# Optimization experiments

Hardware: AMD Instinct MI355X
Metric: run time of the kernel (lower is better)

The kernel has to match this reference:

```python
import jax, jax.numpy as jnp
import numpy as np

CUTOFF = 5.0
ENV_EXP = 5          # envelope_exponent
NUM_RADIAL = 6
EMB = 128
NUM_ATOM_TYPES = 95
N_NODES = 50000
N_EDGES = 800000


def envelope(x):
    # p = exponent + 1
    p = ENV_EXP + 1
    a = -(p + 1) * (p + 2) / 2.0
    b = p * (p + 2) * 1.0
    c = -p * (p + 1) / 2.0
    x_p_0 = x ** (p - 1)
    x_p_1 = x_p_0 * x
    x_p_2 = x_p_1 * x
    return 1.0 / x + a * x_p_0 + b * x_p_1 + c * x_p_2


def setup_inputs() -> dict:
    key = jax.random.key(0)
    ks = jax.random.split(key, 10)
    Z = jax.random.randint(ks[0], (N_NODES,), 0, NUM_ATOM_TYPES)
    src = jax.random.randint(ks[1], (N_EDGES,), 0, N_NODES)
    dst = jax.random.randint(ks[2], (N_EDGES,), 0, N_NODES)
    rbf = jax.random.normal(ks[3], (N_EDGES, NUM_RADIAL), dtype=jnp.float32)
    # distances in (0, cutoff]; keep away from 0 to avoid 1/x blowup
    d = jax.random.uniform(ks[4], (N_EDGES,), dtype=jnp.float32,
                           minval=0.05, maxval=1.0) * CUTOFF
    sqrt3 = float(np.sqrt(3.0))
    emb_table = jax.random.uniform(ks[5], (NUM_ATOM_TYPES, EMB),
                                   dtype=jnp.float32, minval=-sqrt3, maxval=sqrt3)
    W_rbf = jax.random.normal(ks[6], (EMB, NUM_RADIAL), dtype=jnp.float32) * (1.0 / np.sqrt(NUM_RADIAL))
    b_rbf = jnp.zeros((EMB,), dtype=jnp.float32)
    W_dense = jax.random.normal(ks[7], (EMB, 3 * EMB), dtype=jnp.float32) * (1.0 / np.sqrt(3 * EMB))
    b_dense = jnp.zeros((EMB,), dtype=jnp.float32)
    return {"Z": Z, "src": src, "dst": dst, "rbf": rbf, "d": d,
            "emb_table": emb_table, "W_rbf": W_rbf, "b_rbf": b_rbf,
            "W_dense": W_dense, "b_dense": b_dense}


def reference(Z, src, dst, rbf, d, emb_table, W_rbf, b_rbf, W_dense, b_dense):
    act = jax.nn.silu
    # node embeddings: g.ndata['h'] = embedding(Z)
    h = emb_table[Z]                                   # [N, EMB]
    # edge_init
    rbf_proj = act(rbf @ W_rbf.T + b_rbf)              # [E, EMB]
    m = jnp.concatenate([h[src], h[dst], rbf_proj], axis=-1)  # [E, 3*EMB]
    m = act(m @ W_dense.T + b_dense)                   # [E, EMB]
    d_scaled = d / CUTOFF                              # [E]
    # bessel funcs: sin(n*pi*x)/x, n = 1..NUM_RADIAL (stacked along dim=1)
    freqs = jnp.pi * jnp.arange(1, NUM_RADIAL + 1, dtype=d.dtype)  # [R]
    rbf_env = jnp.sin(d_scaled[:, None] * freqs) / d_scaled[:, None]  # [E, R]
    d_cutoff = envelope(d_scaled)                      # [E]
    rbf_env = d_cutoff[:, None] * rbf_env              # [E, R]
    return h, m, rbf_env
```

## Files before the change

kernel.cpp:

```cpp
#include <hip/hip_runtime.h>
#include <hip/hip_bf16.h>
#include <math.h>

#define CUTOFFV 5.0f
#define NRAD 6
#define EMB 128
#define NTYPES 95
#define PI_F 3.14159265358979323846f

typedef short short8 __attribute__((ext_vector_type(8)));
typedef float f32x4 __attribute__((ext_vector_type(4)));
typedef float f32x2 __attribute__((ext_vector_type(2)));

__device__ __forceinline__ unsigned short f2bf(float f) {
    union { float f; unsigned int u; } v; v.f = f;
    unsigned int u = v.u;
    unsigned int r = (u + 0x7FFFu + ((u >> 16) & 1u)) >> 16;
    return (unsigned short)r;
}

__device__ __forceinline__ short bf16s(float f) {
    union { __hip_bfloat16 h; short s; } u;
    u.h = __float2bfloat16(f);
    return u.s;
}

__device__ __forceinline__ float fast_rcp(float x) {
    float y;
    asm("v_rcp_f32 %0, %1" : "=v"(y) : "v"(x));
    return y;
}

__device__ __forceinline__ float silu_f(float x) {
    return x * fast_rcp(1.0f + __expf(-x));
}

__device__ __forceinline__ void lds_barrier() {
    __builtin_amdgcn_sched_barrier(0);
    asm volatile("s_waitcnt lgkmcnt(0)\n\ts_barrier" ::: "memory");
    __builtin_amdgcn_sched_barrier(0);
}

__global__ void prep_kernel(const float* __restrict__ emb,
                            const float* __restrict__ Wd,
                            const float* __restrict__ bd,
                            const float* __restrict__ Wr,
                            const float* __restrict__ brbf,
                            float* __restrict__ P1, float* __restrict__ P2,
                            unsigned short* __restrict__ W3b,
                            float* __restrict__ Wrp) {
    int b = blockIdx.x, tid = threadIdx.x;
    if (b < 2 * NTYPES) {
        int t = b / NTYPES, z = b % NTYPES;
        __shared__ float emb_s[EMB];
        emb_s[tid] = emb[z * EMB + tid];
        __syncthreads();
        float acc = (t == 0) ? bd[tid] : 0.0f;
        const float* wrow = Wd + (size_t)tid * 384 + t * EMB;
        #pragma unroll 8
        for (int j = 0; j < EMB; ++j) acc += emb_s[j] * wrow[j];
        (t == 0 ? P1 : P2)[z * EMB + tid] = acc;
    } else if (b < 2 * NTYPES + 8) {
        int g = (b - 2 * NTYPES) * 128 + tid;
        for (int i = g; i < EMB * EMB; i += 8 * 128) {
            int n = i >> 7, k = i & 127;
            W3b[i] = f2bf(Wd[(size_t)n * 384 + 256 + k]);
        }
    } else {
        if (tid < EMB) {
            int k = tid;
            #pragma unroll
            for (int j = 0; j < 6; ++j) Wrp[k * 8 + j] = Wr[k * 6 + j];
            Wrp[k * 8 + 6] = brbf[k];
            Wrp[k * 8 + 7] = 0.0f;
        }
    }
}

__global__ void h_kernel(const int* __restrict__ Z, const float* __restrict__ emb,
                         float* __restrict__ out_h, int N) {
    int idx = blockIdx.x * 256 + threadIdx.x;
    int total = N * (EMB / 4);
    if (idx >= total) return;
    int v = idx >> 5, c = idx & 31;
    int z = Z[v];
    const f32x4* e4 = (const f32x4*)emb;
    f32x4* o4 = (f32x4*)out_h;
    o4[idx] = e4[z * 32 + c];
}

__global__ void env_kernel(const float* __restrict__ dvec,
                           float* __restrict__ out_env, int E) {
    int e = blockIdx.x * 256 + threadIdx.x;
    if (e >= E) return;
    float x = dvec[e] * (1.0f / CUTOFFV);
    float inv = fast_rcp(x);
    float x2 = x * x;
    float x5 = x2 * x2 * x;
    float env = inv + x5 * (-28.0f + x * (48.0f - 21.0f * x));
    float s1, c1;
    __sincosf(PI_F * x, &s1, &c1);
    float twoc = 2.0f * c1;
    float f = env * inv;
    float s2 = twoc * s1;
    float s3 = twoc * s2 - s1;
    float s4 = twoc * s3 - s2;
    float s5 = twoc * s4 - s3;
    float s6 = twoc * s5 - s4;
    float* o = out_env + (size_t)e * 6;
    __builtin_nontemporal_store((f32x2){f * s1, f * s2}, (f32x2*)o);
    __builtin_nontemporal_store((f32x2){f * s3, f * s4}, (f32x2*)(o + 2));
    __builtin_nontemporal_store((f32x2){f * s5, f * s6}, (f32x2*)(o + 4));
}

__global__ void __launch_bounds__(256, 4)
edge_kernel(const int* __restrict__ Z, const int* __restrict__ src,
            const int* __restrict__ dst, const float* __restrict__ rbf,
            const float* __restrict__ P1, const float* __restrict__ P2,
            const unsigned short* __restrict__ W3b,
            const float* __restrict__ Wrp,
            float* __restrict__ out_m,
            int E, int ntiles) {
    __shared__ unsigned char A_lds[2][64 * 256];
    __shared__ int zs_s[2][64], zd_s[2][64];

    const int tid = threadIdx.x;
    const int lane = tid & 63;
    const int w = tid >> 6;
    const int lr = lane & 15;
    const int lg = lane >> 4;
    const int wu = __builtin_amdgcn_readfirstlane(w);

    short8 wfrag[2][4];
    #pragma unroll
    for (int nt = 0; nt < 2; ++nt) {
        int n = w * 32 + nt * 16 + lr;
        #pragma unroll
        for (int ks = 0; ks < 4; ++ks)
            wfrag[nt][ks] = *(const short8*)(W3b + n * EMB + ks * 32 + lg * 8);
    }

    for (int i = 0; ; ++i) {
        const int tp = blockIdx.x + i * gridDim.x;
        const int tc = tp - gridDim.x;
        const bool do_p = (tp < ntiles);
        const bool do_c = (i > 0) && (tc < ntiles);
        if (!do_p && !do_c) break;
        const int pi = i & 1, ci = pi ^ 1;

        f32x2 ra = {0.f, 0.f}, rb = {0.f, 0.f}, rc = {0.f, 0.f};
        int iv = 0;
        if (do_p) {
            const int e0p = tp * 64;
            int ecl = e0p + lane; if (ecl >= E) ecl = E - 1;
            const f32x2* r2 = (const f32x2*)(rbf + (size_t)ecl * 6);
            ra = r2[0]; rb = r2[1]; rc = r2[2];
            if (tid < 128) {
                int ec = e0p + (tid & 63); if (ec >= E) ec = E - 1;
                iv = (tid < 64) ? src[ec] : dst[ec];
            }
        }

        if (do_c) {
            const int e0c = tc * 64;
            const unsigned char* Ab = A_lds[ci];
            #pragma unroll
            for (int et = 0; et < 4; ++et) {
                const int e_row = et * 16 + lr;
                short8 bfrag[4];
                #pragma unroll
                for (int ks = 0; ks < 4; ++ks) {
                    int off = (e_row * 256 + (ks * 32 + lg * 8) * 2) ^ ((e_row & 7) << 4);
                    bfrag[ks] = *(const short8*)(Ab + off);
                }
                f32x4 acc[2];
                acc[0] = (f32x4){0.f, 0.f, 0.f, 0.f};
                acc[1] = (f32x4){0.f, 0.f, 0.f, 0.f};
                #pragma unroll
                for (int ks = 0; ks < 4; ++ks)
                    #pragma unroll
                    for (int nt = 0; nt < 2; ++nt)
                        acc[nt] = __builtin_amdgcn_mfma_f32_16x16x32_bf16(
                            wfrag[nt][ks], bfrag[ks], acc[nt], 0, 0, 0);

                const int el = e_row;
                const int e = e0c + el;
                const int zs = zs_s[ci][el], zd = zd_s[ci][el];
                #pragma unroll
                for (int nt = 0; nt < 2; ++nt) {
                    int n4 = w * 32 + nt * 16 + lg * 4;
                    const f32x4 p1 = *(const f32x4*)(P1 + zs * EMB + n4);
                    const f32x4 p2 = *(const f32x4*)(P2 + zd * EMB + n4);
                    f32x4 o;
                    o.x = silu_f(acc[nt][0] + p1.x + p2.x);
                    o.y = silu_f(acc[nt][1] + p1.y + p2.y);
                    o.z = silu_f(acc[nt][2] + p1.z + p2.z);
                    o.w = silu_f(acc[nt][3] + p1.w + p2.w);
                    if (e < E)
                        __builtin_nontemporal_store(
                            o, (f32x4*)(out_m + (size_t)e * EMB + n4));
                }
            }
        }

        if (do_p) {
            int zreg = 0;
            if (tid < 128) zreg = Z[iv];

            #pragma unroll
            for (int c = 0; c < 4; ++c) {
                const float* wp0 = Wrp + (size_t)(wu * 32 + c * 8) * 8;
                short8 pk;
                #pragma unroll
                for (int j = 0; j < 8; ++j) {
                    const float* wp = wp0 + j * 8;
                    float pre = wp[6] + ra.x * wp[0] + ra.y * wp[1] +
                                rb.x * wp[2] + rb.y * wp[3] +
                                rc.x * wp[4] + rc.y * wp[5];
                    pk[j] = bf16s(silu_f(pre));
                }
                int k0 = wu * 32 + c * 8;
                int off = (lane * 256 + k0 * 2) ^ ((lane & 7) << 4);
                *(short8*)(A_lds[pi] + off) = pk;
            }

            if (tid < 64) zs_s[pi][tid] = zreg;
            else if (tid < 128) zd_s[pi][tid - 64] = zreg;
        }

        lds_barrier();
    }
}

extern "C" void kernel_launch(void* const* d_in, const int* in_sizes, int n_in,
                              void* d_out, int out_size, void* d_ws, size_t ws_size,
                              hipStream_t stream) {
    const int* Z = (const int*)d_in[0];
    const int* src = (const int*)d_in[1];
    const int* dst = (const int*)d_in[2];
    const float* rbf = (const float*)d_in[3];
    const float* dvec = (const float*)d_in[4];
    const float* emb = (const float*)d_in[5];
    const float* Wr = (const float*)d_in[6];
    const float* brbf = (const float*)d_in[7];
    const float* Wd = (const float*)d_in[8];
    const float* bd = (const float*)d_in[9];

    const int N = in_sizes[0];
    const int E = in_sizes[1];

    float* out_h = (float*)d_out;
    float* out_m = out_h + (size_t)N * EMB;
    float* out_env = out_m + (size_t)E * EMB;

    float* P1 = (float*)d_ws;
    float* P2 = P1 + NTYPES * EMB;
    unsigned short* W3b = (unsigned short*)(P2 + NTYPES * EMB);
    float* Wrp = (float*)(W3b + EMB * EMB);

    prep_kernel<<<2 * NTYPES + 9, 128, 0, stream>>>(emb, Wd, bd, Wr, brbf,
                                                    P1, P2, W3b, Wrp);

    int hblocks = (N * (EMB / 4) + 255) / 256;
    h_kernel<<<hblocks, 256, 0, stream>>>(Z, emb, out_h, N);

    int eblocks = (E + 255) / 256;
    env_kernel<<<eblocks, 256, 0, stream>>>(dvec, out_env, E);

    int ntiles = (E + 63) / 64;
    int grid = ntiles < 1024 ? ntiles : 1024;
    edge_kernel<<<grid, 256, 0, stream>>>(Z, src, dst, rbf,
                                          P1, P2, W3b, Wrp,
                                          out_m, E, ntiles);
}
```

Baseline: 164.3 us.

## Stage MFMA output through LDS for coalesced full-row stores of m

Results of the consume stage are no longer written to global memory straight from the MFMA fragment layout, where each lane stores a scattered 16-byte piece. They are kept in registers, written into the consumed A_lds buffer in two 32-edge passes with an XOR swizzle, then read back so consecutive threads store contiguous 512-byte rows. The aim is better store coalescing for the large output. In exchange it adds LDS traffic, extra barriers per tile and 32 extra live registers, which may reduce occupancy.

```diff
diff --git a/kernel.cpp b/kernel.cpp
--- a/kernel.cpp
+++ b/kernel.cpp
@@ -161,8 +161,8 @@
             }
         }
 
+        f32x4 o[4][2];
         if (do_c) {
-            const int e0c = tc * 64;
             const unsigned char* Ab = A_lds[ci];
             #pragma unroll
             for (int et = 0; et < 4; ++et) {
@@ -184,21 +184,18 @@
                             wfrag[nt][ks], bfrag[ks], acc[nt], 0, 0, 0);
 
                 const int el = e_row;
-                const int e = e0c + el;
                 const int zs = zs_s[ci][el], zd = zd_s[ci][el];
                 #pragma unroll
                 for (int nt = 0; nt < 2; ++nt) {
                     int n4 = w * 32 + nt * 16 + lg * 4;
                     const f32x4 p1 = *(const f32x4*)(P1 + zs * EMB + n4);
                     const f32x4 p2 = *(const f32x4*)(P2 + zd * EMB + n4);
-                    f32x4 o;
-                    o.x = silu_f(acc[nt][0] + p1.x + p2.x);
-                    o.y = silu_f(acc[nt][1] + p1.y + p2.y);
-                    o.z = silu_f(acc[nt][2] + p1.z + p2.z);
-                    o.w = silu_f(acc[nt][3] + p1.w + p2.w);
-                    if (e < E)
-                        __builtin_nontemporal_store(
-                            o, (f32x4*)(out_m + (size_t)e * EMB + n4));
+                    f32x4 v;
+                    v.x = silu_f(acc[nt][0] + p1.x + p2.x);
+                    v.y = silu_f(acc[nt][1] + p1.y + p2.y);
+                    v.z = silu_f(acc[nt][2] + p1.z + p2.z);
+                    v.w = silu_f(acc[nt][3] + p1.w + p2.w);
+                    o[et][nt] = v;
                 }
             }
         }
@@ -229,6 +226,37 @@
         }
 
         lds_barrier();
+
+        if (do_c) {
+            const int e0c = tc * 64;
+            unsigned char* Sb = (unsigned char*)A_lds[ci];
+            #pragma unroll
+            for (int p = 0; p < 2; ++p) {
+                #pragma unroll
+                for (int q = 0; q < 2; ++q) {
+                    const int epass = q * 16 + lr;
+                    const int swz = (lr & 7) << 4;
+                    #pragma unroll
+                    for (int nt = 0; nt < 2; ++nt) {
+                        int addr = epass * 512 + ((w * 128 + nt * 64 + lg * 16) ^ swz);
+                        *(f32x4*)(Sb + addr) = o[2 * p + q][nt];
+                    }
+                }
+                lds_barrier();
+                #pragma unroll
+                for (int s = 0; s < 4; ++s) {
+                    const int epass = s * 8 + (tid >> 5);
+                    const int within = (tid & 31) * 16;
+                    const int rd = epass * 512 + (within ^ ((epass & 7) << 4));
+                    f32x4 v = *(const f32x4*)(Sb + rd);
+                    const int ge = e0c + p * 32 + epass;
+                    if (ge < E)
+                        __builtin_nontemporal_store(
+                            v, (f32x4*)(out_m + (size_t)ge * EMB + (tid & 31) * 4));
+                }
+                lds_barrier();
+            }
+        }
     }
 }
 
```

After: 154.8 us. 1.06x faster.
